# Kernel tuning notes

Measured on AMD Instinct MI355X. Metric: run time of the kernel, lower is better.

## Reference

```python
import jax, jax.numpy as jnp
import numpy as np

H = 64   # hidden_layers
D = 1    # frame_dimension
N = 2048 # n_samples (batch)
T = 512  # seq_len


def setup_inputs() -> dict:
    key = jax.random.key(0)
    ks = jax.random.split(key, 12)
    s = 1.0 / np.sqrt(H)
    u = lambda k, shape: jax.random.uniform(k, shape, jnp.float32, -s, s)
    return {
        "y": jax.random.normal(ks[0], (N, T), dtype=jnp.float32),
        "W_ih1": u(ks[1], (4 * H, D)),
        "W_hh1": u(ks[2], (4 * H, H)),
        "b_ih1": u(ks[3], (4 * H,)),
        "b_hh1": u(ks[4], (4 * H,)),
        "W_ih2": u(ks[5], (4 * H, H)),
        "W_hh2": u(ks[6], (4 * H, H)),
        "b_ih2": u(ks[7], (4 * H,)),
        "b_hh2": u(ks[8], (4 * H,)),
        "W_lin": u(ks[9], (D, H)),
        "b_lin": u(ks[10], (D,)),
        "pre_output_len": 1,
    }


def _lstm_cell(x, h, c, W_ih, W_hh, b_ih, b_hh):
    # gates in PyTorch LSTMCell order: input, forget, cell(g), output
    g = x @ W_ih.T + b_ih + h @ W_hh.T + b_hh  # [n, 4H]
    i, f, gg, o = jnp.split(g, 4, axis=-1)
    i = jax.nn.sigmoid(i)
    f = jax.nn.sigmoid(f)
    gg = jnp.tanh(gg)
    o = jax.nn.sigmoid(o)
    c2 = f * c + i * gg
    h2 = o * jnp.tanh(c2)
    return h2, c2


def reference(y, W_ih1, W_hh1, b_ih1, b_hh1, W_ih2, W_hh2, b_ih2, b_hh2,
              W_lin, b_lin, pre_output_len):
    n = y.shape[0]
    zeros = jnp.zeros((n, H), dtype=jnp.float32)
    init = (zeros, zeros, zeros, zeros)

    def step(carry, x_t):
        h1, c1, h2, c2 = carry
        h1, c1 = _lstm_cell(x_t, h1, c1, W_ih1, W_hh1, b_ih1, b_hh1)
        h2, c2 = _lstm_cell(h1, h2, c2, W_ih2, W_hh2, b_ih2, b_hh2)
        out = h2 @ W_lin.T + b_lin  # [n, D]
        return (h1, c1, h2, c2), out

    ys = jnp.swapaxes(y, 0, 1)[:, :, None]  # [T, n, 1]
    _, outs = jax.lax.scan(step, init, ys)  # [T, n, D]
    outs = outs[pre_output_len:]            # drop first pre_output_len steps (static)
    # torch.cat along dim=1 of [n, D] chunks -> [n, (T - pre)*D]
    return jnp.transpose(outs, (1, 0, 2)).reshape(n, -1)
```

## Files before the change

kernel.cpp:

```cpp
#include <hip/hip_runtime.h>


typedef __attribute__((ext_vector_type(8))) short short8;
typedef __attribute__((ext_vector_type(4))) float f32x4;

#define NT 512
#define XPITCH 2060
#define XP 0
#define HP 32960
#define RING 51392
#define LDS_BYTES 84160
#define PLANE(layer, buf, hl) (HP + ((((layer) * 2 + (buf)) * 2) + (hl)) * 2304)
#define L2E 1.44269504f
#define N2L2E (-2.8853900817779268f)

__device__ __forceinline__ float fast_rcp(float x) { return __builtin_amdgcn_rcpf(x); }
__device__ __forceinline__ float exp2_f(float x) {
  float r; asm("v_exp_f32 %0, %1" : "=v"(r) : "v"(x)); return r;
}
__device__ __forceinline__ unsigned short bf_rne(float f) {
  unsigned u = __float_as_uint(f);
  return (unsigned short)((u + 0x7FFFu + ((u >> 16) & 1u)) >> 16);
}
__device__ __forceinline__ void split8sc(const float* p, float sc, short8& hi, short8& lo) {
#pragma unroll
  for (int e = 0; e < 8; ++e) {
    float v = p[e] * sc;
    unsigned short h = bf_rne(v);
    float hf = __uint_as_float(((unsigned)h) << 16);
    hi[e] = (short)h;
    lo[e] = (short)bf_rne(v - hf);
  }
}
__device__ __forceinline__ unsigned cvt_pk(float a, float b) {
  unsigned r;
  asm("v_cvt_pk_bf16_f32 %0, %1, %2" : "=v"(r) : "v"(a), "v"(b));
  return r;
}
__device__ __forceinline__ f32x4 mfma16(short8 a, short8 b, f32x4 c) {
  return __builtin_amdgcn_mfma_f32_16x16x32_bf16(a, b, c, 0, 0, 0);
}
__device__ __forceinline__ void cell2(float i, float f, float g, float o,
                                      float& c, float& h) {
  const float ei = exp2_f(-i), ef = exp2_f(-f), eg = exp2_f(-g), eo = exp2_f(-o);
  const float P = (1.f - eg) * fast_rcp((1.f + ei) * (1.f + eg));
  c = fmaf(c, fast_rcp(1.f + ef), P);
  const float cc = fminf(15.f, fmaxf(-15.f, c));
  const float ec = exp2_f(N2L2E * cc);
  h = (1.f - ec) * fast_rcp((1.f + eo) * (1.f + ec));
}

__global__ __launch_bounds__(512, 2) void lstm2_r13(
    const float* __restrict__ y, const float* __restrict__ Wih1,
    const float* __restrict__ Whh1, const float* __restrict__ bih1,
    const float* __restrict__ bhh1, const float* __restrict__ Wih2,
    const float* __restrict__ Whh2, const float* __restrict__ bih2,
    const float* __restrict__ bhh2, const float* __restrict__ Wlin,
    const float* __restrict__ blin, float* __restrict__ out) {
  extern __shared__ char smem[];
  const int tid = threadIdx.x;
  const int w = tid >> 6;
  const int lane = tid & 63;
  const int g = lane >> 4;
  const int s = lane & 15;
  const int s0 = blockIdx.x * 16;

  for (int i = tid; i < 16 * 512; i += 512) {
    const int ss = i >> 9, t = i & 511;
    *(float*)(smem + XP + ss * XPITCH + t * 4) = y[(size_t)(s0 + ss) * 512 + t];
  }
  for (int i = tid; i < 18432 / 4; i += 512) *(float*)(smem + HP + i * 4) = 0.f;
  const float bl0 = blin[0];
  __syncthreads();

  const int bo0 = s * 144 + 16 * g, bo1 = bo0 + 64;
  const float gsc[4] = {L2E, L2E, 2.0f * L2E, L2E};

  if (w < 4) {
    short8 a1h[4][2], a1l[4][2];
#pragma unroll
    for (int p = 0; p < 4; ++p)
#pragma unroll
      for (int c = 0; c < 2; ++c)
        split8sc(Whh1 + (size_t)(p * 64 + 16 * w + s) * 64 + 32 * c + 8 * g,
                 gsc[p], a1h[p][c], a1l[p][c]);
    float bias1c[4][4], wih1c[4][4];
#pragma unroll
    for (int p = 0; p < 4; ++p)
#pragma unroll
      for (int r = 0; r < 4; ++r) {
        const int row = p * 64 + 16 * w + 4 * g + r;
        bias1c[p][r] = (bih1[row] + bhh1[row]) * gsc[p];
        wih1c[p][r] = Wih1[row] * gsc[p];
      }
    float c1[4] = {0.f, 0.f, 0.f, 0.f};
    const int hwr0 = s * 144 + 32 * w + 8 * g;

    int eR[2][4], eW[2][2];
#pragma unroll
    for (int P = 0; P < 2; ++P) {
      const int rb = P ^ 1;
      eR[P][0] = PLANE(0, rb, 0) + bo0;
      eR[P][1] = PLANE(0, rb, 1) + bo0;
      eR[P][2] = PLANE(0, rb, 0) + bo1;
      eR[P][3] = PLANE(0, rb, 1) + bo1;
      eW[P][0] = PLANE(0, P, 0) + hwr0;
      eW[P][1] = PLANE(0, P, 1) + hwr0;
    }

#define EBODY(KK, P)                                                          \
  {                                                                           \
    const float x = *(const float*)(smem + XP + s * XPITCH + (KK) * 4);       \
    const short8 Bh0 = *(const short8*)(smem + eR[P][0]);                     \
    const short8 Bl0 = *(const short8*)(smem + eR[P][1]);                     \
    const short8 Bh1 = *(const short8*)(smem + eR[P][2]);                     \
    const short8 Bl1 = *(const short8*)(smem + eR[P][3]);                     \
    f32x4 acc[4];                                                             \
    _Pragma("unroll") for (int p = 0; p < 4; ++p) {                           \
      _Pragma("unroll") for (int r = 0; r < 4; ++r)                           \
          acc[p][r] = fmaf(wih1c[p][r], x, bias1c[p][r]);                     \
    }                                                                         \
    __builtin_amdgcn_s_setprio(1);                                            \
    _Pragma("unroll") for (int p = 0; p < 4; ++p)                             \
        acc[p] = mfma16(a1h[p][0], Bh0, acc[p]);                              \
    _Pragma("unroll") for (int p = 0; p < 4; ++p)                             \
        acc[p] = mfma16(a1h[p][1], Bh1, acc[p]);                              \
    _Pragma("unroll") for (int p = 0; p < 4; ++p)                             \
        acc[p] = mfma16(a1h[p][0], Bl0, acc[p]);                              \
    _Pragma("unroll") for (int p = 0; p < 4; ++p)                             \
        acc[p] = mfma16(a1h[p][1], Bl1, acc[p]);                              \
    _Pragma("unroll") for (int p = 0; p < 4; ++p)                             \
        acc[p] = mfma16(a1l[p][0], Bh0, acc[p]);                              \
    _Pragma("unroll") for (int p = 0; p < 4; ++p)                             \
        acc[p] = mfma16(a1l[p][1], Bh1, acc[p]);                              \
    __builtin_amdgcn_s_setprio(0);                                            \
    float h1n[4];                                                             \
    _Pragma("unroll") for (int r = 0; r < 4; ++r)                             \
        cell2(acc[0][r], acc[1][r], acc[2][r], acc[3][r], c1[r], h1n[r]);     \
    const unsigned hA = cvt_pk(h1n[0], h1n[1]), hB = cvt_pk(h1n[2], h1n[3]);  \
    const unsigned lA = cvt_pk(h1n[0] - __uint_as_float(hA << 16),            \
                               h1n[1] - __uint_as_float(hA & 0xFFFF0000u));   \
    const unsigned lB = cvt_pk(h1n[2] - __uint_as_float(hB << 16),            \
                               h1n[3] - __uint_as_float(hB & 0xFFFF0000u));   \
    *(uint2*)(smem + eW[P][0]) = make_uint2(hA, hB);                          \
    *(uint2*)(smem + eW[P][1]) = make_uint2(lA, lB);                          \
  }

    EBODY(0, 0);
    __syncthreads();
#pragma unroll 1
    for (int kb = 1; kb <= 509; kb += 2) {
      EBODY(kb, 1);
      __syncthreads();
      EBODY(kb + 1, 0);
      __syncthreads();
    }
    EBODY(511, 1);
    __syncthreads();
    __syncthreads();
  } else {
    const int ow = w - 4;
    short8 a2h[4][4], a2l[4][4];
#pragma unroll
    for (int p = 0; p < 4; ++p)
#pragma unroll
      for (int c = 0; c < 4; ++c) {
        const float* src = (c < 2)
            ? (Wih2 + (size_t)(p * 64 + 16 * ow + s) * 64 + 32 * c + 8 * g)
            : (Whh2 + (size_t)(p * 64 + 16 * ow + s) * 64 + 32 * (c - 2) + 8 * g);
        split8sc(src, gsc[p], a2h[p][c], a2l[p][c]);
      }
    f32x4 bias2v[4];
    float wlinc[4];
#pragma unroll
    for (int p = 0; p < 4; ++p)
#pragma unroll
      for (int r = 0; r < 4; ++r) {
        const int row = p * 64 + 16 * ow + 4 * g + r;
        bias2v[p][r] = (bih2[row] + bhh2[row]) * gsc[p];
      }
#pragma unroll
    for (int r = 0; r < 4; ++r) wlinc[r] = Wlin[16 * ow + 4 * g + r];
    float c2[4] = {0.f, 0.f, 0.f, 0.f};
    const int hwr0 = s * 144 + 32 * ow + 8 * g;
    const int ringb = RING + ow * 64 + s * 4;

    int oR[2][8], oW[2][2];
#pragma unroll
    for (int P = 0; P < 2; ++P) {
      oR[P][0] = PLANE(0, P ^ 1, 0) + bo0;
      oR[P][1] = PLANE(0, P ^ 1, 1) + bo0;
      oR[P][2] = PLANE(0, P ^ 1, 0) + bo1;
      oR[P][3] = PLANE(0, P ^ 1, 1) + bo1;
      oR[P][4] = PLANE(1, P, 0) + bo0;
      oR[P][5] = PLANE(1, P, 1) + bo0;
      oR[P][6] = PLANE(1, P, 0) + bo1;
      oR[P][7] = PLANE(1, P, 1) + bo1;
      oW[P][0] = PLANE(1, P ^ 1, 0) + hwr0;
      oW[P][1] = PLANE(1, P ^ 1, 1) + hwr0;
    }

#define OFLUSH(KK)                                                            \
  if ((KK) >= 66 && (((KK)-2) & 63) == 0) {                                   \
    const int base = (KK)-66;                                                 \
    const int thr = ow * 64 + lane;                                           \
    const int ss2 = thr & 15, grp = thr >> 4;                                 \
    _Pragma("unroll") for (int q = 0; q < 4; ++q) {                           \
      const int idx = base + grp * 4 + q;                                     \
      const char* op = smem + RING + (idx & 127) * 256 + ss2 * 4;             \
      const float v = *(const float*)(op) + *(const float*)(op + 64) +        \
                      *(const float*)(op + 128) + *(const float*)(op + 192) + \
                      bl0;                                                    \
      out[(size_t)(s0 + ss2) * 511 + idx] = v;                                \
    }                                                                         \
  }

#define OBODY(KK, P)                                                          \
  {                                                                           \
    const short8 Bh0 = *(const short8*)(smem + oR[P][0]);                     \
    const short8 Bl0 = *(const short8*)(smem + oR[P][1]);                     \
    const short8 Bh1 = *(const short8*)(smem + oR[P][2]);                     \
    const short8 Bl1 = *(const short8*)(smem + oR[P][3]);                     \
    const short8 Ch0 = *(const short8*)(smem + oR[P][4]);                     \
    const short8 Cl0 = *(const short8*)(smem + oR[P][5]);                     \
    const short8 Ch1 = *(const short8*)(smem + oR[P][6]);                     \
    const short8 Cl1 = *(const short8*)(smem + oR[P][7]);                     \
    f32x4 acc[4];                                                             \
    __builtin_amdgcn_s_setprio(1);                                            \
    _Pragma("unroll") for (int p = 0; p < 4; ++p)                             \
        acc[p] = mfma16(a2h[p][0], Bh0, bias2v[p]);                           \
    _Pragma("unroll") for (int p = 0; p < 4; ++p)                             \
        acc[p] = mfma16(a2h[p][1], Bh1, acc[p]);                              \
    _Pragma("unroll") for (int p = 0; p < 4; ++p)                             \
        acc[p] = mfma16(a2h[p][0], Bl0, acc[p]);                              \
    _Pragma("unroll") for (int p = 0; p < 4; ++p)                             \
        acc[p] = mfma16(a2h[p][1], Bl1, acc[p]);                              \
    _Pragma("unroll") for (int p = 0; p < 4; ++p)                             \
        acc[p] = mfma16(a2l[p][0], Bh0, acc[p]);                              \
    _Pragma("unroll") for (int p = 0; p < 4; ++p)                             \
        acc[p] = mfma16(a2l[p][1], Bh1, acc[p]);                              \
    _Pragma("unroll") for (int p = 0; p < 4; ++p)                             \
        acc[p] = mfma16(a2h[p][2], Ch0, acc[p]);                              \
    _Pragma("unroll") for (int p = 0; p < 4; ++p)                             \
        acc[p] = mfma16(a2h[p][3], Ch1, acc[p]);                              \
    _Pragma("unroll") for (int p = 0; p < 4; ++p)                             \
        acc[p] = mfma16(a2h[p][2], Cl0, acc[p]);                              \
    _Pragma("unroll") for (int p = 0; p < 4; ++p)                             \
        acc[p] = mfma16(a2h[p][3], Cl1, acc[p]);                              \
    _Pragma("unroll") for (int p = 0; p < 4; ++p)                             \
        acc[p] = mfma16(a2l[p][2], Ch0, acc[p]);                              \
    _Pragma("unroll") for (int p = 0; p < 4; ++p)                             \
        acc[p] = mfma16(a2l[p][3], Ch1, acc[p]);                              \
    __builtin_amdgcn_s_setprio(0);                                            \
    float h2n[4];                                                             \
    _Pragma("unroll") for (int r = 0; r < 4; ++r)                             \
        cell2(acc[0][r], acc[1][r], acc[2][r], acc[3][r], c2[r], h2n[r]);     \
    const unsigned hA = cvt_pk(h2n[0], h2n[1]), hB = cvt_pk(h2n[2], h2n[3]);  \
    const unsigned lA = cvt_pk(h2n[0] - __uint_as_float(hA << 16),            \
                               h2n[1] - __uint_as_float(hA & 0xFFFF0000u));   \
    const unsigned lB = cvt_pk(h2n[2] - __uint_as_float(hB << 16),            \
                               h2n[3] - __uint_as_float(hB & 0xFFFF0000u));   \
    *(uint2*)(smem + oW[P][0]) = make_uint2(hA, hB);                          \
    *(uint2*)(smem + oW[P][1]) = make_uint2(lA, lB);                          \
    if ((KK) >= 2) {                                                          \
      float pw = wlinc[0] * h2n[0];                                           \
      pw = fmaf(wlinc[1], h2n[1], pw);                                        \
      pw = fmaf(wlinc[2], h2n[2], pw);                                        \
      pw = fmaf(wlinc[3], h2n[3], pw);                                        \
      pw += __shfl_xor(pw, 16, 64);                                           \
      pw += __shfl_xor(pw, 32, 64);                                           \
      if (g == 0)                                                             \
        *(float*)(smem + ringb + (((KK)-2) & 127) * 256) = pw;                \
    }                                                                         \
  }

    __syncthreads();
#pragma unroll 1
    for (int kb = 1; kb <= 509; kb += 2) {
      OBODY(kb, 1);
      __syncthreads();
      OFLUSH(kb + 1);
      OBODY(kb + 1, 0);
      __syncthreads();
    }
    OBODY(511, 1);
    __syncthreads();
    OBODY(512, 0);
    __syncthreads();
    {
      const int thr = ow * 64 + lane;
      for (int e = thr; e < 63 * 16; e += 256) {
        const int ss2 = e & 15, off = e >> 4;
        const int idx = 448 + off;
        const char* op = smem + RING + (idx & 127) * 256 + ss2 * 4;
        const float v = *(const float*)(op) + *(const float*)(op + 64) +
                        *(const float*)(op + 128) + *(const float*)(op + 192) + bl0;
        out[(size_t)(s0 + ss2) * 511 + idx] = v;
      }
    }
  }
}

extern "C" void kernel_launch(void* const* d_in, const int* in_sizes, int n_in,
                              void* d_out, int out_size, void* d_ws, size_t ws_size,
                              hipStream_t stream) {
  const float* y    = (const float*)d_in[0];
  const float* Wih1 = (const float*)d_in[1];
  const float* Whh1 = (const float*)d_in[2];
  const float* bih1 = (const float*)d_in[3];
  const float* bhh1 = (const float*)d_in[4];
  const float* Wih2 = (const float*)d_in[5];
  const float* Whh2 = (const float*)d_in[6];
  const float* bih2 = (const float*)d_in[7];
  const float* bhh2 = (const float*)d_in[8];
  const float* Wlin = (const float*)d_in[9];
  const float* blin = (const float*)d_in[10];
  float* out = (float*)d_out;

  hipFuncSetAttribute((const void*)lstm2_r13,
                      hipFuncAttributeMaxDynamicSharedMemorySize, LDS_BYTES);
  lstm2_r13<<<dim3(128), dim3(512), LDS_BYTES, stream>>>(
      y, Wih1, Whh1, bih1, bhh1, Wih2, Whh2, bih2, bhh2, Wlin, blin, out);
}
```

Before: 636.3 us.

## Rebalance layer-2 input projection onto layer-1 warps with deeper pipelining

```diff
diff --git a/kernel.cpp b/kernel.cpp
--- a/kernel.cpp
+++ b/kernel.cpp
@@ -4,13 +4,15 @@
 typedef __attribute__((ext_vector_type(8))) short short8;
 typedef __attribute__((ext_vector_type(4))) float f32x4;
 
-#define NT 512
 #define XPITCH 2060
 #define XP 0
-#define HP 32960
-#define RING 51392
-#define LDS_BYTES 84160
-#define PLANE(layer, buf, hl) (HP + ((((layer) * 2 + (buf)) * 2) + (hl)) * 2304)
+#define H1B 32960
+#define H1(S, HL) (H1B + (S) * 4608 + (HL) * 2304)
+#define H2B 51392
+#define H2(Q, HL) (H2B + (Q) * 4608 + (HL) * 2304)
+#define PBB 60608
+#define RING 101568
+#define LDS_BYTES 134336
 #define L2E 1.44269504f
 #define N2L2E (-2.8853900817779268f)
 
@@ -50,7 +52,7 @@
   h = (1.f - ec) * fast_rcp((1.f + eo) * (1.f + ec));
 }
 
-__global__ __launch_bounds__(512, 2) void lstm2_r13(
+__global__ __launch_bounds__(512, 2) void lstm2_r14(
     const float* __restrict__ y, const float* __restrict__ Wih1,
     const float* __restrict__ Whh1, const float* __restrict__ bih1,
     const float* __restrict__ bhh1, const float* __restrict__ Wih2,
@@ -69,52 +71,48 @@
     const int ss = i >> 9, t = i & 511;
     *(float*)(smem + XP + ss * XPITCH + t * 4) = y[(size_t)(s0 + ss) * 512 + t];
   }
-  for (int i = tid; i < 18432 / 4; i += 512) *(float*)(smem + HP + i * 4) = 0.f;
+  for (int i = tid; i < 27648 / 4; i += 512)
+    *(float*)(smem + H1B + i * 4) = 0.f;
   const float bl0 = blin[0];
   __syncthreads();
 
   const int bo0 = s * 144 + 16 * g, bo1 = bo0 + 64;
   const float gsc[4] = {L2E, L2E, 2.0f * L2E, L2E};
+  const f32x4 zero4 = {0.f, 0.f, 0.f, 0.f};
 
   if (w < 4) {
-    short8 a1h[4][2], a1l[4][2];
+    const int row = 16 * w + s;
+    short8 a1h[4][2], a1l[4][2], aPh[4], aPl[4];
+#pragma unroll
+    for (int p = 0; p < 4; ++p) {
+#pragma unroll
+      for (int c = 0; c < 2; ++c)
+        split8sc(Whh1 + (size_t)(p * 64 + row) * 64 + 32 * c + 8 * g, gsc[p],
+                 a1h[p][c], a1l[p][c]);
+      split8sc(Wih2 + (size_t)(p * 64 + row) * 64 + 8 * g, gsc[p], aPh[p], aPl[p]);
+    }
+    float bias1c[4][4], wih1c[4][4];
 #pragma unroll
     for (int p = 0; p < 4; ++p)
 #pragma unroll
-      for (int c = 0; c < 2; ++c)
-        split8sc(Whh1 + (size_t)(p * 64 + 16 * w + s) * 64 + 32 * c + 8 * g,
-                 gsc[p], a1h[p][c], a1l[p][c]);
-    float bias1c[4][4], wih1c[4][4];
-#pragma unroll
-    for (int p = 0; p < 4; ++p)
-#pragma unroll
       for (int r = 0; r < 4; ++r) {
-        const int row = p * 64 + 16 * w + 4 * g + r;
-        bias1c[p][r] = (bih1[row] + bhh1[row]) * gsc[p];
-        wih1c[p][r] = Wih1[row] * gsc[p];
+        const int rr = p * 64 + 16 * w + 4 * g + r;
+        bias1c[p][r] = (bih1[rr] + bhh1[rr]) * gsc[p];
+        wih1c[p][r] = Wih1[rr] * gsc[p];
       }
     float c1[4] = {0.f, 0.f, 0.f, 0.f};
     const int hwr0 = s * 144 + 32 * w + 8 * g;
-
-    int eR[2][4], eW[2][2];
-#pragma unroll
-    for (int P = 0; P < 2; ++P) {
-      const int rb = P ^ 1;
-      eR[P][0] = PLANE(0, rb, 0) + bo0;
-      eR[P][1] = PLANE(0, rb, 1) + bo0;
-      eR[P][2] = PLANE(0, rb, 0) + bo1;
-      eR[P][3] = PLANE(0, rb, 1) + bo1;
-      eW[P][0] = PLANE(0, P, 0) + hwr0;
-      eW[P][1] = PLANE(0, P, 1) + hwr0;
-    }
-
-#define EBODY(KK, P)                                                          \
+    const float* xrow = (const float*)(smem + XP + s * XPITCH);
+    char* pb0 = smem + PBB + w * 1280 + lane * 16 + (lane >> 3) * 16;
+    char* pb1 = pb0 + 20480;
+
+#define EB(KK, S)                                                             \
   {                                                                           \
-    const float x = *(const float*)(smem + XP + s * XPITCH + (KK) * 4);       \
-    const short8 Bh0 = *(const short8*)(smem + eR[P][0]);                     \
-    const short8 Bl0 = *(const short8*)(smem + eR[P][1]);                     \
-    const short8 Bh1 = *(const short8*)(smem + eR[P][2]);                     \
-    const short8 Bl1 = *(const short8*)(smem + eR[P][3]);                     \
+    const float x = xrow[KK];                                                 \
+    const short8 Bh0 = *(const short8*)(smem + H1(((S) + 3) & 3, 0) + bo0);   \
+    const short8 Bl0 = *(const short8*)(smem + H1(((S) + 3) & 3, 1) + bo0);   \
+    const short8 Bh1 = *(const short8*)(smem + H1(((S) + 3) & 3, 0) + bo1);   \
+    const short8 Bl1 = *(const short8*)(smem + H1(((S) + 3) & 3, 1) + bo1);   \
     f32x4 acc[4];                                                             \
     _Pragma("unroll") for (int p = 0; p < 4; ++p) {                           \
       _Pragma("unroll") for (int r = 0; r < 4; ++r)                           \
@@ -133,6 +131,18 @@
         acc[p] = mfma16(a1l[p][0], Bh0, acc[p]);                              \
     _Pragma("unroll") for (int p = 0; p < 4; ++p)                             \
         acc[p] = mfma16(a1l[p][1], Bh1, acc[p]);                              \
+    if ((KK) >= 1) {                                                          \
+      f32x4 ap[4];                                                            \
+      _Pragma("unroll") for (int p = 0; p < 4; ++p)                           \
+          ap[p] = mfma16(aPl[p], Bh0, zero4);                                 \
+      _Pragma("unroll") for (int p = 0; p < 4; ++p)                           \
+          ap[p] = mfma16(aPh[p], Bl0, ap[p]);                                 \
+      _Pragma("unroll") for (int p = 0; p < 4; ++p)                           \
+          ap[p] = mfma16(aPh[p], Bh0, ap[p]);                                 \
+      char* pw = ((((S) + 1) & 1) ? pb1 : pb0);                               \
+      _Pragma("unroll") for (int p = 0; p < 4; ++p)                           \
+          *(f32x4*)(pw + p * 5120) = ap[p];                                   \
+    }                                                                         \
     __builtin_amdgcn_s_setprio(0);                                            \
     float h1n[4];                                                             \
     _Pragma("unroll") for (int r = 0; r < 4; ++r)                             \
@@ -142,67 +152,69 @@
                                h1n[1] - __uint_as_float(hA & 0xFFFF0000u));   \
     const unsigned lB = cvt_pk(h1n[2] - __uint_as_float(hB << 16),            \
                                h1n[3] - __uint_as_float(hB & 0xFFFF0000u));   \
-    *(uint2*)(smem + eW[P][0]) = make_uint2(hA, hB);                          \
-    *(uint2*)(smem + eW[P][1]) = make_uint2(lA, lB);                          \
-  }
-
-    EBODY(0, 0);
-    __syncthreads();
+    *(uint2*)(smem + H1((S), 0) + hwr0) = make_uint2(hA, hB);                 \
+    *(uint2*)(smem + H1((S), 1) + hwr0) = make_uint2(lA, lB);                 \
+  }
+
 #pragma unroll 1
-    for (int kb = 1; kb <= 509; kb += 2) {
-      EBODY(kb, 1);
-      __syncthreads();
-      EBODY(kb + 1, 0);
-      __syncthreads();
-    }
-    EBODY(511, 1);
+    for (int kb = 0; kb < 512; kb += 4) {
+      EB(kb + 0, 0);
+      __syncthreads();
+      EB(kb + 1, 1);
+      __syncthreads();
+      EB(kb + 2, 2);
+      __syncthreads();
+      EB(kb + 3, 3);
+      __syncthreads();
+    }
+    {
+      const short8 Bh0 = *(const short8*)(smem + H1(3, 0) + bo0);
+      const short8 Bl0 = *(const short8*)(smem + H1(3, 1) + bo0);
+      f32x4 ap[4];
+#pragma unroll
+      for (int p = 0; p < 4; ++p) ap[p] = mfma16(aPl[p], Bh0, zero4);
+#pragma unroll
+      for (int p = 0; p < 4; ++p) ap[p] = mfma16(aPh[p], Bl0, ap[p]);
+#pragma unroll
+      for (int p = 0; p < 4; ++p) ap[p] = mfma16(aPh[p], Bh0, ap[p]);
+#pragma unroll
+      for (int p = 0; p < 4; ++p) *(f32x4*)(pb1 + p * 5120) = ap[p];
+    }
     __syncthreads();
     __syncthreads();
   } else {
     const int ow = w - 4;
-    short8 a2h[4][4], a2l[4][4];
-#pragma unroll
-    for (int p = 0; p < 4; ++p)
-#pragma unroll
-      for (int c = 0; c < 4; ++c) {
-        const float* src = (c < 2)
-            ? (Wih2 + (size_t)(p * 64 + 16 * ow + s) * 64 + 32 * c + 8 * g)
-            : (Whh2 + (size_t)(p * 64 + 16 * ow + s) * 64 + 32 * (c - 2) + 8 * g);
-        split8sc(src, gsc[p], a2h[p][c], a2l[p][c]);
-      }
+    const int row = 16 * ow + s;
+    short8 a2h1[4], a2l1[4], ahh[4][2], all_[4][2];
+#pragma unroll
+    for (int p = 0; p < 4; ++p) {
+      split8sc(Wih2 + (size_t)(p * 64 + row) * 64 + 32 + 8 * g, gsc[p],
+               a2h1[p], a2l1[p]);
+#pragma unroll
+      for (int c = 0; c < 2; ++c)
+        split8sc(Whh2 + (size_t)(p * 64 + row) * 64 + 32 * c + 8 * g, gsc[p],
+                 ahh[p][c], all_[p][c]);
+    }
     f32x4 bias2v[4];
     float wlinc[4];
 #pragma unroll
     for (int p = 0; p < 4; ++p)
 #pragma unroll
       for (int r = 0; r < 4; ++r) {
-        const int row = p * 64 + 16 * ow + 4 * g + r;
-        bias2v[p][r] = (bih2[row] + bhh2[row]) * gsc[p];
+        const int rr = p * 64 + 16 * ow + 4 * g + r;
+        bias2v[p][r] = (bih2[rr] + bhh2[rr]) * gsc[p];
       }
 #pragma unroll
     for (int r = 0; r < 4; ++r) wlinc[r] = Wlin[16 * ow + 4 * g + r];
     float c2[4] = {0.f, 0.f, 0.f, 0.f};
     const int hwr0 = s * 144 + 32 * ow + 8 * g;
-    const int ringb = RING + ow * 64 + s * 4;
-
-    int oR[2][8], oW[2][2];
-#pragma unroll
-    for (int P = 0; P < 2; ++P) {
-      oR[P][0] = PLANE(0, P ^ 1, 0) + bo0;
-      oR[P][1] = PLANE(0, P ^ 1, 1) + bo0;
-      oR[P][2] = PLANE(0, P ^ 1, 0) + bo1;
-      oR[P][3] = PLANE(0, P ^ 1, 1) + bo1;
-      oR[P][4] = PLANE(1, P, 0) + bo0;
-      oR[P][5] = PLANE(1, P, 1) + bo0;
-      oR[P][6] = PLANE(1, P, 0) + bo1;
-      oR[P][7] = PLANE(1, P, 1) + bo1;
-      oW[P][0] = PLANE(1, P ^ 1, 0) + hwr0;
-      oW[P][1] = PLANE(1, P ^ 1, 1) + hwr0;
-    }
+    const char* po0 = smem + PBB + ow * 1280 + lane * 16 + (lane >> 3) * 16;
+    const char* po1 = po0 + 20480;
+    char* ringb = smem + RING + ow * 64 + s * 4;
 
 #define OFLUSH(KK)                                                            \
-  if ((KK) >= 66 && (((KK)-2) & 63) == 0) {                                   \
-    const int base = (KK)-66;                                                 \
+  if ((KK) >= 67 && (((KK) - 3) & 63) == 0) {                                 \
+    const int base = (KK) - 67;                                               \
     const int thr = ow * 64 + lane;                                           \
     const int ss2 = thr & 15, grp = thr >> 4;                                 \
     _Pragma("unroll") for (int q = 0; q < 4; ++q) {                           \
@@ -215,77 +227,82 @@
     }                                                                         \
   }
 
-#define OBODY(KK, P)                                                          \
+#define OB(KK, S)                                                             \
   {                                                                           \
-    const short8 Bh0 = *(const short8*)(smem + oR[P][0]);                     \
-    const short8 Bl0 = *(const short8*)(smem + oR[P][1]);                     \
-    const short8 Bh1 = *(const short8*)(smem + oR[P][2]);                     \
-    const short8 Bl1 = *(const short8*)(smem + oR[P][3]);                     \
-    const short8 Ch0 = *(const short8*)(smem + oR[P][4]);                     \
-    const short8 Cl0 = *(const short8*)(smem + oR[P][5]);                     \
-    const short8 Ch1 = *(const short8*)(smem + oR[P][6]);                     \
-    const short8 Cl1 = *(const short8*)(smem + oR[P][7]);                     \
-    f32x4 acc[4];                                                             \
-    __builtin_amdgcn_s_setprio(1);                                            \
-    _Pragma("unroll") for (int p = 0; p < 4; ++p)                             \
-        acc[p] = mfma16(a2h[p][0], Bh0, bias2v[p]);                           \
-    _Pragma("unroll") for (int p = 0; p < 4; ++p)                             \
-        acc[p] = mfma16(a2h[p][1], Bh1, acc[p]);                              \
-    _Pragma("unroll") for (int p = 0; p < 4; ++p)                             \
-        acc[p] = mfma16(a2h[p][0], Bl0, acc[p]);                              \
-    _Pragma("unroll") for (int p = 0; p < 4; ++p)                             \
-        acc[p] = mfma16(a2h[p][1], Bl1, acc[p]);                              \
-    _Pragma("unroll") for (int p = 0; p < 4; ++p)                             \
-        acc[p] = mfma16(a2l[p][0], Bh0, acc[p]);                              \
-    _Pragma("unroll") for (int p = 0; p < 4; ++p)                             \
-        acc[p] = mfma16(a2l[p][1], Bh1, acc[p]);                              \
-    _Pragma("unroll") for (int p = 0; p < 4; ++p)                             \
-        acc[p] = mfma16(a2h[p][2], Ch0, acc[p]);                              \
-    _Pragma("unroll") for (int p = 0; p < 4; ++p)                             \
-        acc[p] = mfma16(a2h[p][3], Ch1, acc[p]);                              \
-    _Pragma("unroll") for (int p = 0; p < 4; ++p)                             \
-        acc[p] = mfma16(a2h[p][2], Cl0, acc[p]);                              \
-    _Pragma("unroll") for (int p = 0; p < 4; ++p)                             \
-        acc[p] = mfma16(a2h[p][3], Cl1, acc[p]);                              \
-    _Pragma("unroll") for (int p = 0; p < 4; ++p)                             \
-        acc[p] = mfma16(a2l[p][2], Ch0, acc[p]);                              \
-    _Pragma("unroll") for (int p = 0; p < 4; ++p)                             \
-        acc[p] = mfma16(a2l[p][3], Ch1, acc[p]);                              \
-    __builtin_amdgcn_s_setprio(0);                                            \
-    float h2n[4];                                                             \
-    _Pragma("unroll") for (int r = 0; r < 4; ++r)                             \
-        cell2(acc[0][r], acc[1][r], acc[2][r], acc[3][r], c2[r], h2n[r]);     \
-    const unsigned hA = cvt_pk(h2n[0], h2n[1]), hB = cvt_pk(h2n[2], h2n[3]);  \
-    const unsigned lA = cvt_pk(h2n[0] - __uint_as_float(hA << 16),            \
-                               h2n[1] - __uint_as_float(hA & 0xFFFF0000u));   \
-    const unsigned lB = cvt_pk(h2n[2] - __uint_as_float(hB << 16),            \
-                               h2n[3] - __uint_as_float(hB & 0xFFFF0000u));   \
-    *(uint2*)(smem + oW[P][0]) = make_uint2(hA, hB);                          \
-    *(uint2*)(smem + oW[P][1]) = make_uint2(lA, lB);                          \
+    OFLUSH(KK);                                                               \
     if ((KK) >= 2) {                                                          \
-      float pw = wlinc[0] * h2n[0];                                           \
-      pw = fmaf(wlinc[1], h2n[1], pw);                                        \
-      pw = fmaf(wlinc[2], h2n[2], pw);                                        \
-      pw = fmaf(wlinc[3], h2n[3], pw);                                        \
-      pw += __shfl_xor(pw, 16, 64);                                           \
-      pw += __shfl_xor(pw, 32, 64);                                           \
-      if (g == 0)                                                             \
-        *(float*)(smem + ringb + (((KK)-2) & 127) * 256) = pw;                \
+      const char* pr = (((S) & 1) ? po1 : po0);                               \
+      f32x4 pa[4];                                                            \
+      _Pragma("unroll") for (int p = 0; p < 4; ++p)                           \
+          pa[p] = *(const f32x4*)(pr + p * 5120);                             \
+      const short8 Bh1 = *(const short8*)(smem + H1(((S) + 2) & 3, 0) + bo1); \
+      const short8 Bl1 = *(const short8*)(smem + H1(((S) + 2) & 3, 1) + bo1); \
+      const short8 Ch0 = *(const short8*)(smem + H2(((S) + 1) & 1, 0) + bo0); \
+      const short8 Cl0 = *(const short8*)(smem + H2(((S) + 1) & 1, 1) + bo0); \
+      const short8 Ch1 = *(const short8*)(smem + H2(((S) + 1) & 1, 0) + bo1); \
+      const short8 Cl1 = *(const short8*)(smem + H2(((S) + 1) & 1, 1) + bo1); \
+      f32x4 acc[4], acx[4];                                                   \
+      __builtin_amdgcn_s_setprio(1);                                          \
+      _Pragma("unroll") for (int p = 0; p < 4; ++p)                           \
+          acc[p] = mfma16(a2h1[p], Bh1, bias2v[p]);                           \
+      _Pragma("unroll") for (int p = 0; p < 4; ++p)                           \
+          acx[p] = mfma16(ahh[p][0], Ch0, zero4);                             \
+      _Pragma("unroll") for (int p = 0; p < 4; ++p)                           \
+          acc[p] = mfma16(a2h1[p], Bl1, acc[p]);                              \
+      _Pragma("unroll") for (int p = 0; p < 4; ++p)                           \
+          acx[p] = mfma16(ahh[p][1], Ch1, acx[p]);                            \
+      _Pragma("unroll") for (int p = 0; p < 4; ++p)                           \
+          acc[p] = mfma16(a2l1[p], Bh1, acc[p]);                              \
+      _Pragma("unroll") for (int p = 0; p < 4; ++p)                           \
+          acx[p] = mfma16(ahh[p][0], Cl0, acx[p]);                            \
+      _Pragma("unroll") for (int p = 0; p < 4; ++p)                           \
+          acc[p] = mfma16(all_[p][0], Ch0, acc[p]);                           \
+      _Pragma("unroll") for (int p = 0; p < 4; ++p)                           \
+          acx[p] = mfma16(ahh[p][1], Cl1, acx[p]);                            \
+      _Pragma("unroll") for (int p = 0; p < 4; ++p)                           \
+          acc[p] = mfma16(all_[p][1], Ch1, acc[p]);                           \
+      __builtin_amdgcn_s_setprio(0);                                          \
+      float h2n[4];                                                           \
+      _Pragma("unroll") for (int r = 0; r < 4; ++r) {                         \
+        const float gi = acc[0][r] + acx[0][r] + pa[0][r];                    \
+        const float gf = acc[1][r] + acx[1][r] + pa[1][r];                    \
+        const float gg = acc[2][r] + acx[2][r] + pa[2][r];                    \
+        const float go = acc[3][r] + acx[3][r] + pa[3][r];                    \
+        cell2(gi, gf, gg, go, c2[r], h2n[r]);                                 \
+      }                                                                       \
+      const unsigned hA = cvt_pk(h2n[0], h2n[1]), hB = cvt_pk(h2n[2], h2n[3]);\
+      const unsigned lA = cvt_pk(h2n[0] - __uint_as_float(hA << 16),          \
+                                 h2n[1] - __uint_as_float(hA & 0xFFFF0000u)); \
+      const unsigned lB = cvt_pk(h2n[2] - __uint_as_float(hB << 16),          \
+                                 h2n[3] - __uint_as_float(hB & 0xFFFF0000u)); \
+      *(uint2*)(smem + H2((S) & 1, 0) + hwr0) = make_uint2(hA, hB);           \
+      *(uint2*)(smem + H2((S) & 1, 1) + hwr0) = make_uint2(lA, lB);           \
+      if ((KK) >= 3) {                                                        \
+        float pw = wlinc[0] * h2n[0];                                         \
+        pw = fmaf(wlinc[1], h2n[1], pw);                                      \
+        pw = fmaf(wlinc[2], h2n[2], pw);                                      \
+        pw = fmaf(wlinc[3], h2n[3], pw);                                      \
+        pw += __shfl_xor(pw, 16, 64);                                         \
+        pw += __shfl_xor(pw, 32, 64);                                         \
+        if (g == 0) *(float*)(ringb + (((KK) - 3) & 127) * 256) = pw;         \
+      }                                                                       \
     }                                                                         \
   }
 
+#pragma unroll 1
+    for (int kb = 0; kb < 512; kb += 4) {
+      OB(kb + 0, 0);
+      __syncthreads();
+      OB(kb + 1, 1);
+      __syncthreads();
+      OB(kb + 2, 2);
+      __syncthreads();
+      OB(kb + 3, 3);
+      __syncthreads();
+    }
+    OB(512, 0);
     __syncthreads();
-#pragma unroll 1
-    for (int kb = 1; kb <= 509; kb += 2) {
-      OBODY(kb, 1);
-      __syncthreads();
-      OFLUSH(kb + 1);
-      OBODY(kb + 1, 0);
-      __syncthreads();
-    }
-    OBODY(511, 1);
-    __syncthreads();
-    OBODY(512, 0);
+    OB(513, 1);
     __syncthreads();
     {
       const int thr = ow * 64 + lane;
@@ -317,8 +334,8 @@
   const float* blin = (const float*)d_in[10];
   float* out = (float*)d_out;
 
-  hipFuncSetAttribute((const void*)lstm2_r13,
+  hipFuncSetAttribute((const void*)lstm2_r14,
                       hipFuncAttributeMaxDynamicSharedMemorySize, LDS_BYTES);
-  lstm2_r13<<<dim3(128), dim3(512), LDS_BYTES, stream>>>(
+  lstm2_r14<<<dim3(128), dim3(512), LDS_BYTES, stream>>>(
       y, Wih1, Whh1, bih1, bhh1, Wih2, Whh2, bih2, bhh2, Wlin, blin, out);
 }
```

After: 643.4 us. No clear change (+1.1%).

## Replace split-bf16 MFMA recurrence with two-level int8 fixed-point MFMA

Applied to the files above, without the earlier changes.

```diff
diff --git a/kernel.cpp b/kernel.cpp
--- a/kernel.cpp
+++ b/kernel.cpp
@@ -1,16 +1,15 @@
 #include <hip/hip_runtime.h>
 
 
-typedef __attribute__((ext_vector_type(8))) short short8;
+typedef __attribute__((ext_vector_type(4))) int i32x4;
 typedef __attribute__((ext_vector_type(4))) float f32x4;
 
-#define NT 512
 #define XPITCH 2060
 #define XP 0
-#define HP 32960
-#define RING 51392
-#define LDS_BYTES 84160
-#define PLANE(layer, buf, hl) (HP + ((((layer) * 2 + (buf)) * 2) + (hl)) * 2304)
+#define HB 32960
+#define HPL(layer, P, L) (HB + ((((layer) * 2 + (P)) * 2) + (L)) * 1280)
+#define RING 43200
+#define LDS_BYTES 75968
 #define L2E 1.44269504f
 #define N2L2E (-2.8853900817779268f)
 
@@ -18,27 +17,8 @@
 __device__ __forceinline__ float exp2_f(float x) {
   float r; asm("v_exp_f32 %0, %1" : "=v"(r) : "v"(x)); return r;
 }
-__device__ __forceinline__ unsigned short bf_rne(float f) {
-  unsigned u = __float_as_uint(f);
-  return (unsigned short)((u + 0x7FFFu + ((u >> 16) & 1u)) >> 16);
-}
-__device__ __forceinline__ void split8sc(const float* p, float sc, short8& hi, short8& lo) {
-#pragma unroll
-  for (int e = 0; e < 8; ++e) {
-    float v = p[e] * sc;
-    unsigned short h = bf_rne(v);
-    float hf = __uint_as_float(((unsigned)h) << 16);
-    hi[e] = (short)h;
-    lo[e] = (short)bf_rne(v - hf);
-  }
-}
-__device__ __forceinline__ unsigned cvt_pk(float a, float b) {
-  unsigned r;
-  asm("v_cvt_pk_bf16_f32 %0, %1, %2" : "=v"(r) : "v"(a), "v"(b));
-  return r;
-}
-__device__ __forceinline__ f32x4 mfma16(short8 a, short8 b, f32x4 c) {
-  return __builtin_amdgcn_mfma_f32_16x16x32_bf16(a, b, c, 0, 0, 0);
+__device__ __forceinline__ i32x4 mfma_i8(i32x4 a, i32x4 b, i32x4 c) {
+  return __builtin_amdgcn_mfma_i32_16x16x64_i8(a, b, c, 0, 0, 0);
 }
 __device__ __forceinline__ void cell2(float i, float f, float g, float o,
                                       float& c, float& h) {
@@ -49,8 +29,42 @@
   const float ec = exp2_f(N2L2E * cc);
   h = (1.f - ec) * fast_rcp((1.f + eo) * (1.f + ec));
 }
-
-__global__ __launch_bounds__(512, 2) void lstm2_r13(
+__device__ __forceinline__ void quantW16(const float* p, i32x4& w0v, i32x4& w1v) {
+  int b0[16], b1[16];
+#pragma unroll
+  for (int e = 0; e < 16; ++e) {
+    const float v = p[e];
+    const float q0 = rintf(v * 512.f);
+    const float r = v - q0 * (1.f / 512.f);
+    const float q1 = fminf(127.f, fmaxf(-127.f, rintf(r * 131072.f)));
+    b0[e] = (int)q0;
+    b1[e] = (int)q1;
+  }
+#pragma unroll
+  for (int d = 0; d < 4; ++d) {
+    w0v[d] = (b0[4 * d] & 255) | ((b0[4 * d + 1] & 255) << 8) |
+             ((b0[4 * d + 2] & 255) << 16) | ((b0[4 * d + 3] & 255) << 24);
+    w1v[d] = (b1[4 * d] & 255) | ((b1[4 * d + 1] & 255) << 8) |
+             ((b1[4 * d + 2] & 255) << 16) | ((b1[4 * d + 3] & 255) << 24);
+  }
+}
+__device__ __forceinline__ void quantH4(const float* h, unsigned& L0, unsigned& L1) {
+  int q0[4], q1[4];
+#pragma unroll
+  for (int r = 0; r < 4; ++r) {
+    const float q0f = rintf(h[r] * 64.f);
+    q0[r] = (int)q0f;
+    const float rr = h[r] - q0f * 0.015625f;
+    const float q1f = fminf(127.f, fmaxf(-127.f, rintf(rr * 16384.f)));
+    q1[r] = (int)q1f;
+  }
+  L0 = (q0[0] & 255) | ((q0[1] & 255) << 8) | ((q0[2] & 255) << 16) |
+       ((q0[3] & 255) << 24);
+  L1 = (q1[0] & 255) | ((q1[1] & 255) << 8) | ((q1[2] & 255) << 16) |
+       ((q1[3] & 255) << 24);
+}
+
+__global__ __launch_bounds__(512, 2) void lstm2_r15(
     const float* __restrict__ y, const float* __restrict__ Wih1,
     const float* __restrict__ Whh1, const float* __restrict__ bih1,
     const float* __restrict__ bhh1, const float* __restrict__ Wih2,
@@ -69,136 +83,104 @@
     const int ss = i >> 9, t = i & 511;
     *(float*)(smem + XP + ss * XPITCH + t * 4) = y[(size_t)(s0 + ss) * 512 + t];
   }
-  for (int i = tid; i < 18432 / 4; i += 512) *(float*)(smem + HP + i * 4) = 0.f;
+  for (int i = tid; i < 10240 / 4; i += 512) *(float*)(smem + HB + i * 4) = 0.f;
   const float bl0 = blin[0];
   __syncthreads();
 
-  const int bo0 = s * 144 + 16 * g, bo1 = bo0 + 64;
+  const int boff = s * 80 + 16 * g;
   const float gsc[4] = {L2E, L2E, 2.0f * L2E, L2E};
+  const i32x4 zeroi = {0, 0, 0, 0};
+  float sc00[4], scB[4];
+#pragma unroll
+  for (int p = 0; p < 4; ++p) {
+    sc00[p] = gsc[p] * (1.f / 32768.f);
+    scB[p] = gsc[p] * (1.f / 8388608.f);
+  }
 
   if (w < 4) {
-    short8 a1h[4][2], a1l[4][2];
+    const int row = 16 * w + s;
+    i32x4 aW0[4], aW1[4];
 #pragma unroll
     for (int p = 0; p < 4; ++p)
-#pragma unroll
-      for (int c = 0; c < 2; ++c)
-        split8sc(Whh1 + (size_t)(p * 64 + 16 * w + s) * 64 + 32 * c + 8 * g,
-                 gsc[p], a1h[p][c], a1l[p][c]);
+      quantW16(Whh1 + (size_t)(p * 64 + row) * 64 + 16 * g, aW0[p], aW1[p]);
     float bias1c[4][4], wih1c[4][4];
 #pragma unroll
     for (int p = 0; p < 4; ++p)
 #pragma unroll
       for (int r = 0; r < 4; ++r) {
-        const int row = p * 64 + 16 * w + 4 * g + r;
-        bias1c[p][r] = (bih1[row] + bhh1[row]) * gsc[p];
-        wih1c[p][r] = Wih1[row] * gsc[p];
+        const int rr = p * 64 + 16 * w + 4 * g + r;
+        bias1c[p][r] = (bih1[rr] + bhh1[rr]) * gsc[p];
+        wih1c[p][r] = Wih1[rr] * gsc[p];
       }
     float c1[4] = {0.f, 0.f, 0.f, 0.f};
-    const int hwr0 = s * 144 + 32 * w + 8 * g;
-
-    int eR[2][4], eW[2][2];
-#pragma unroll
-    for (int P = 0; P < 2; ++P) {
-      const int rb = P ^ 1;
-      eR[P][0] = PLANE(0, rb, 0) + bo0;
-      eR[P][1] = PLANE(0, rb, 1) + bo0;
-      eR[P][2] = PLANE(0, rb, 0) + bo1;
-      eR[P][3] = PLANE(0, rb, 1) + bo1;
-      eW[P][0] = PLANE(0, P, 0) + hwr0;
-      eW[P][1] = PLANE(0, P, 1) + hwr0;
-    }
-
-#define EBODY(KK, P)                                                          \
+    const int hwA = s * 80 + 16 * w + 4 * g;
+    const float* xrow = (const float*)(smem + XP + s * XPITCH);
+
+#define EB(KK, P)                                                             \
   {                                                                           \
-    const float x = *(const float*)(smem + XP + s * XPITCH + (KK) * 4);       \
-    const short8 Bh0 = *(const short8*)(smem + eR[P][0]);                     \
-    const short8 Bl0 = *(const short8*)(smem + eR[P][1]);                     \
-    const short8 Bh1 = *(const short8*)(smem + eR[P][2]);                     \
-    const short8 Bl1 = *(const short8*)(smem + eR[P][3]);                     \
-    f32x4 acc[4];                                                             \
+    const float x = xrow[KK];                                                 \
+    const i32x4 B0 = *(const i32x4*)(smem + HPL(0, (P) ^ 1, 0) + boff);       \
+    const i32x4 B1 = *(const i32x4*)(smem + HPL(0, (P) ^ 1, 1) + boff);       \
+    i32x4 S00[4], SB[4];                                                      \
+    __builtin_amdgcn_s_setprio(1);                                            \
+    _Pragma("unroll") for (int p = 0; p < 4; ++p)                             \
+        S00[p] = mfma_i8(aW0[p], B0, zeroi);                                  \
+    _Pragma("unroll") for (int p = 0; p < 4; ++p)                             \
+        SB[p] = mfma_i8(aW1[p], B0, zeroi);                                   \
+    _Pragma("unroll") for (int p = 0; p < 4; ++p)                             \
+        SB[p] = mfma_i8(aW0[p], B1, SB[p]);                                   \
+    __builtin_amdgcn_s_setprio(0);                                            \
+    float ga[4][4];                                                           \
     _Pragma("unroll") for (int p = 0; p < 4; ++p) {                           \
-      _Pragma("unroll") for (int r = 0; r < 4; ++r)                           \
-          acc[p][r] = fmaf(wih1c[p][r], x, bias1c[p][r]);                     \
-    }                                                                         \
-    __builtin_amdgcn_s_setprio(1);                                            \
-    _Pragma("unroll") for (int p = 0; p < 4; ++p)                             \
-        acc[p] = mfma16(a1h[p][0], Bh0, acc[p]);                              \
-    _Pragma("unroll") for (int p = 0; p < 4; ++p)                             \
-        acc[p] = mfma16(a1h[p][1], Bh1, acc[p]);                              \
-    _Pragma("unroll") for (int p = 0; p < 4; ++p)                             \
-        acc[p] = mfma16(a1h[p][0], Bl0, acc[p]);                              \
-    _Pragma("unroll") for (int p = 0; p < 4; ++p)                             \
-        acc[p] = mfma16(a1h[p][1], Bl1, acc[p]);                              \
-    _Pragma("unroll") for (int p = 0; p < 4; ++p)                             \
-        acc[p] = mfma16(a1l[p][0], Bh0, acc[p]);                              \
-    _Pragma("unroll") for (int p = 0; p < 4; ++p)                             \
-        acc[p] = mfma16(a1l[p][1], Bh1, acc[p]);                              \
-    __builtin_amdgcn_s_setprio(0);                                            \
+      _Pragma("unroll") for (int r = 0; r < 4; ++r) {                         \
+        float base = fmaf(wih1c[p][r], x, bias1c[p][r]);                      \
+        base = fmaf((float)SB[p][r], scB[p], base);                           \
+        ga[p][r] = fmaf((float)S00[p][r], sc00[p], base);                     \
+      }                                                                       \
+    }                                                                         \
     float h1n[4];                                                             \
     _Pragma("unroll") for (int r = 0; r < 4; ++r)                             \
-        cell2(acc[0][r], acc[1][r], acc[2][r], acc[3][r], c1[r], h1n[r]);     \
-    const unsigned hA = cvt_pk(h1n[0], h1n[1]), hB = cvt_pk(h1n[2], h1n[3]);  \
-    const unsigned lA = cvt_pk(h1n[0] - __uint_as_float(hA << 16),            \
-                               h1n[1] - __uint_as_float(hA & 0xFFFF0000u));   \
-    const unsigned lB = cvt_pk(h1n[2] - __uint_as_float(hB << 16),            \
-                               h1n[3] - __uint_as_float(hB & 0xFFFF0000u));   \
-    *(uint2*)(smem + eW[P][0]) = make_uint2(hA, hB);                          \
-    *(uint2*)(smem + eW[P][1]) = make_uint2(lA, lB);                          \
-  }
-
-    EBODY(0, 0);
+        cell2(ga[0][r], ga[1][r], ga[2][r], ga[3][r], c1[r], h1n[r]);         \
+    unsigned L0, L1;                                                          \
+    quantH4(h1n, L0, L1);                                                     \
+    *(unsigned*)(smem + HPL(0, (P), 0) + hwA) = L0;                           \
+    *(unsigned*)(smem + HPL(0, (P), 1) + hwA) = L1;                           \
+  }
+
+    EB(0, 0);
     __syncthreads();
 #pragma unroll 1
     for (int kb = 1; kb <= 509; kb += 2) {
-      EBODY(kb, 1);
-      __syncthreads();
-      EBODY(kb + 1, 0);
-      __syncthreads();
-    }
-    EBODY(511, 1);
+      EB(kb, 1);
+      __syncthreads();
+      EB(kb + 1, 0);
+      __syncthreads();
+    }
+    EB(511, 1);
     __syncthreads();
     __syncthreads();
   } else {
     const int ow = w - 4;
-    short8 a2h[4][4], a2l[4][4];
+    const int row = 16 * ow + s;
+    i32x4 bW0[4], bW1[4], cW0[4], cW1[4];
+#pragma unroll
+    for (int p = 0; p < 4; ++p) {
+      quantW16(Wih2 + (size_t)(p * 64 + row) * 64 + 16 * g, bW0[p], bW1[p]);
+      quantW16(Whh2 + (size_t)(p * 64 + row) * 64 + 16 * g, cW0[p], cW1[p]);
+    }
+    float bias2c[4][4], wlinc[4];
 #pragma unroll
     for (int p = 0; p < 4; ++p)
 #pragma unroll
-      for (int c = 0; c < 4; ++c) {
-        const float* src = (c < 2)
-            ? (Wih2 + (size_t)(p * 64 + 16 * ow + s) * 64 + 32 * c + 8 * g)
-            : (Whh2 + (size_t)(p * 64 + 16 * ow + s) * 64 + 32 * (c - 2) + 8 * g);
-        split8sc(src, gsc[p], a2h[p][c], a2l[p][c]);
-      }
-    f32x4 bias2v[4];
-    float wlinc[4];
-#pragma unroll
-    for (int p = 0; p < 4; ++p)
-#pragma unroll
       for (int r = 0; r < 4; ++r) {
-        const int row = p * 64 + 16 * ow + 4 * g + r;
-        bias2v[p][r] = (bih2[row] + bhh2[row]) * gsc[p];
+        const int rr = p * 64 + 16 * ow + 4 * g + r;
+        bias2c[p][r] = (bih2[rr] + bhh2[rr]) * gsc[p];
       }
 #pragma unroll
     for (int r = 0; r < 4; ++r) wlinc[r] = Wlin[16 * ow + 4 * g + r];
     float c2[4] = {0.f, 0.f, 0.f, 0.f};
-    const int hwr0 = s * 144 + 32 * ow + 8 * g;
-    const int ringb = RING + ow * 64 + s * 4;
-
-    int oR[2][8], oW[2][2];
-#pragma unroll
-    for (int P = 0; P < 2; ++P) {
-      oR[P][0] = PLANE(0, P ^ 1, 0) + bo0;
-      oR[P][1] = PLANE(0, P ^ 1, 1) + bo0;
-      oR[P][2] = PLANE(0, P ^ 1, 0) + bo1;
-      oR[P][3] = PLANE(0, P ^ 1, 1) + bo1;
-      oR[P][4] = PLANE(1, P, 0) + bo0;
-      oR[P][5] = PLANE(1, P, 1) + bo0;
-      oR[P][6] = PLANE(1, P, 0) + bo1;
-      oR[P][7] = PLANE(1, P, 1) + bo1;
-      oW[P][0] = PLANE(1, P ^ 1, 0) + hwr0;
-      oW[P][1] = PLANE(1, P ^ 1, 1) + hwr0;
-    }
+    const int hwA = s * 80 + 16 * ow + 4 * g;
+    char* ringb = smem + RING + ow * 64 + s * 4;
 
 #define OFLUSH(KK)                                                            \
   if ((KK) >= 66 && (((KK)-2) & 63) == 0) {                                   \
@@ -215,53 +197,41 @@
     }                                                                         \
   }
 
-#define OBODY(KK, P)                                                          \
+#define OB(KK, P)                                                             \
   {                                                                           \
-    const short8 Bh0 = *(const short8*)(smem + oR[P][0]);                     \
-    const short8 Bl0 = *(const short8*)(smem + oR[P][1]);                     \
-    const short8 Bh1 = *(const short8*)(smem + oR[P][2]);                     \
-    const short8 Bl1 = *(const short8*)(smem + oR[P][3]);                     \
-    const short8 Ch0 = *(const short8*)(smem + oR[P][4]);                     \
-    const short8 Cl0 = *(const short8*)(smem + oR[P][5]);                     \
-    const short8 Ch1 = *(const short8*)(smem + oR[P][6]);                     \
-    const short8 Cl1 = *(const short8*)(smem + oR[P][7]);                     \
-    f32x4 acc[4];                                                             \
+    const i32x4 B10 = *(const i32x4*)(smem + HPL(0, (P) ^ 1, 0) + boff);      \
+    const i32x4 B11 = *(const i32x4*)(smem + HPL(0, (P) ^ 1, 1) + boff);      \
+    const i32x4 B20 = *(const i32x4*)(smem + HPL(1, (P), 0) + boff);          \
+    const i32x4 B21 = *(const i32x4*)(smem + HPL(1, (P), 1) + boff);          \
+    i32x4 S00[4], SB[4];                                                      \
     __builtin_amdgcn_s_setprio(1);                                            \
     _Pragma("unroll") for (int p = 0; p < 4; ++p)                             \
-        acc[p] = mfma16(a2h[p][0], Bh0, bias2v[p]);                           \
-    _Pragma("unroll") for (int p = 0; p < 4; ++p)                             \
-        acc[p] = mfma16(a2h[p][1], Bh1, acc[p]);                              \
-    _Pragma("unroll") for (int p = 0; p < 4; ++p)                             \
-        acc[p] = mfma16(a2h[p][0], Bl0, acc[p]);                              \
-    _Pragma("unroll") for (int p = 0; p < 4; ++p)                             \
-        acc[p] = mfma16(a2h[p][1], Bl1, acc[p]);                              \
-    _Pragma("unroll") for (int p = 0; p < 4; ++p)                             \
-        acc[p] = mfma16(a2l[p][0], Bh0, acc[p]);                              \
-    _Pragma("unroll") for (int p = 0; p < 4; ++p)                             \
-        acc[p] = mfma16(a2l[p][1], Bh1, acc[p]);                              \
-    _Pragma("unroll") for (int p = 0; p < 4; ++p)                             \
-        acc[p] = mfma16(a2h[p][2], Ch0, acc[p]);                              \
-    _Pragma("unroll") for (int p = 0; p < 4; ++p)                             \
-        acc[p] = mfma16(a2h[p][3], Ch1, acc[p]);                              \
-    _Pragma("unroll") for (int p = 0; p < 4; ++p)                             \
-        acc[p] = mfma16(a2h[p][2], Cl0, acc[p]);                              \
-    _Pragma("unroll") for (int p = 0; p < 4; ++p)                             \
-        acc[p] = mfma16(a2h[p][3], Cl1, acc[p]);                              \
-    _Pragma("unroll") for (int p = 0; p < 4; ++p)                             \
-        acc[p] = mfma16(a2l[p][2], Ch0, acc[p]);                              \
-    _Pragma("unroll") for (int p = 0; p < 4; ++p)                             \
-        acc[p] = mfma16(a2l[p][3], Ch1, acc[p]);                              \
+        S00[p] = mfma_i8(bW0[p], B10, zeroi);                                 \
+    _Pragma("unroll") for (int p = 0; p < 4; ++p)                             \
+        SB[p] = mfma_i8(bW1[p], B10, zeroi);                                  \
+    _Pragma("unroll") for (int p = 0; p < 4; ++p)                             \
+        S00[p] = mfma_i8(cW0[p], B20, S00[p]);                                \
+    _Pragma("unroll") for (int p = 0; p < 4; ++p)                             \
+        SB[p] = mfma_i8(bW0[p], B11, SB[p]);                                  \
+    _Pragma("unroll") for (int p = 0; p < 4; ++p)                             \
+        SB[p] = mfma_i8(cW1[p], B20, SB[p]);                                  \
+    _Pragma("unroll") for (int p = 0; p < 4; ++p)                             \
+        SB[p] = mfma_i8(cW0[p], B21, SB[p]);                                  \
     __builtin_amdgcn_s_setprio(0);                                            \
+    float ga[4][4];                                                           \
+    _Pragma("unroll") for (int p = 0; p < 4; ++p) {                           \
+      _Pragma("unroll") for (int r = 0; r < 4; ++r) {                         \
+        float base = fmaf((float)SB[p][r], scB[p], bias2c[p][r]);             \
+        ga[p][r] = fmaf((float)S00[p][r], sc00[p], base);                     \
+      }                                                                       \
+    }                                                                         \
     float h2n[4];                                                             \
     _Pragma("unroll") for (int r = 0; r < 4; ++r)                             \
-        cell2(acc[0][r], acc[1][r], acc[2][r], acc[3][r], c2[r], h2n[r]);     \
-    const unsigned hA = cvt_pk(h2n[0], h2n[1]), hB = cvt_pk(h2n[2], h2n[3]);  \
-    const unsigned lA = cvt_pk(h2n[0] - __uint_as_float(hA << 16),            \
-                               h2n[1] - __uint_as_float(hA & 0xFFFF0000u));   \
-    const unsigned lB = cvt_pk(h2n[2] - __uint_as_float(hB << 16),            \
-                               h2n[3] - __uint_as_float(hB & 0xFFFF0000u));   \
-    *(uint2*)(smem + oW[P][0]) = make_uint2(hA, hB);                          \
-    *(uint2*)(smem + oW[P][1]) = make_uint2(lA, lB);                          \
+        cell2(ga[0][r], ga[1][r], ga[2][r], ga[3][r], c2[r], h2n[r]);         \
+    unsigned L0, L1;                                                          \
+    quantH4(h2n, L0, L1);                                                     \
+    *(unsigned*)(smem + HPL(1, (P) ^ 1, 0) + hwA) = L0;                       \
+    *(unsigned*)(smem + HPL(1, (P) ^ 1, 1) + hwA) = L1;                       \
     if ((KK) >= 2) {                                                          \
       float pw = wlinc[0] * h2n[0];                                           \
       pw = fmaf(wlinc[1], h2n[1], pw);                                        \
@@ -269,23 +239,22 @@
       pw = fmaf(wlinc[3], h2n[3], pw);                                        \
       pw += __shfl_xor(pw, 16, 64);                                           \
       pw += __shfl_xor(pw, 32, 64);                                           \
-      if (g == 0)                                                             \
-        *(float*)(smem + ringb + (((KK)-2) & 127) * 256) = pw;                \
+      if (g == 0) *(float*)(ringb + (((KK)-2) & 127) * 256) = pw;             \
     }                                                                         \
   }
 
     __syncthreads();
 #pragma unroll 1
     for (int kb = 1; kb <= 509; kb += 2) {
-      OBODY(kb, 1);
+      OB(kb, 1);
       __syncthreads();
       OFLUSH(kb + 1);
-      OBODY(kb + 1, 0);
-      __syncthreads();
-    }
-    OBODY(511, 1);
-    __syncthreads();
-    OBODY(512, 0);
+      OB(kb + 1, 0);
+      __syncthreads();
+    }
+    OB(511, 1);
+    __syncthreads();
+    OB(512, 0);
     __syncthreads();
     {
       const int thr = ow * 64 + lane;
@@ -317,8 +286,8 @@
   const float* blin = (const float*)d_in[10];
   float* out = (float*)d_out;
 
-  hipFuncSetAttribute((const void*)lstm2_r13,
+  hipFuncSetAttribute((const void*)lstm2_r15,
                       hipFuncAttributeMaxDynamicSharedMemorySize, LDS_BYTES);
-  lstm2_r13<<<dim3(128), dim3(512), LDS_BYTES, stream>>>(
+  lstm2_r15<<<dim3(128), dim3(512), LDS_BYTES, stream>>>(
       y, Wih1, Whh1, bih1, bhh1, Wih2, Whh2, bih2, bhh2, Wlin, blin, out);
 }
```

Result: faster. 564.9 us (-11.2%).
